# Kernel tuning notes

Hardware: AMD Instinct MI355X
Metric: run time of the kernel (lower is better)

The kernel has to match this reference:

```python
import jax, jax.numpy as jnp
import numpy as np
from jax import lax

# ---- static config (matches init_kwargs) ----
ORDER = 1
NPTS = ORDER + 1            # 2
JUNC_K = 300
LINE_K = 5000
NMS_SIZE = 3
JUNC_THRESH = 0.008
EPS = 1e-5
B, C, H, W = 4, 256, 160, 160
HID = C // 4                # 64
OUT_CH = [1, 1, 2, 1, 2, 4]  # lmap,jmap,joff,cmap,coff,lvec
NHEADS = len(OUT_CH)
MAXO = max(OUT_CH)          # pad conv2 out-channels to 4 per head
# channel-select indices from padded (NHEADS*MAXO) grouped-conv output
SEL = np.array([h * MAXO + c for h, k in enumerate(OUT_CH) for c in range(k)])
# lvec channel permutation from original forward (identity for order=1)
PERM = np.arange(OUT_CH[-1]).reshape(-1, 2, 2)
PERM[:, 1] = PERM[::-1, 1]
PERM = PERM.reshape(-1)


def setup_inputs() -> dict:
    key = jax.random.key(0)
    ks = jax.random.split(key, 9)
    features = jax.random.normal(ks[0], (B, C, H, W), jnp.float32)
    w1 = jax.random.normal(ks[1], (NHEADS * HID, C, 3, 3), jnp.float32) / np.sqrt(C * 9)
    b1 = 0.01 * jax.random.normal(ks[2], (NHEADS * HID,), jnp.float32)
    gamma = 1.0 + 0.1 * jax.random.normal(ks[3], (NHEADS * HID,), jnp.float32)
    beta = 0.01 * jax.random.normal(ks[4], (NHEADS * HID,), jnp.float32)
    mean = 0.1 * jax.random.normal(ks[5], (NHEADS * HID,), jnp.float32)
    var = jax.random.uniform(ks[6], (NHEADS * HID,), jnp.float32, 0.5, 1.5)
    w2 = jax.random.normal(ks[7], (NHEADS * MAXO, HID, 3, 3), jnp.float32) / np.sqrt(HID * 9)
    b2 = 0.01 * jax.random.normal(ks[8], (NHEADS * MAXO,), jnp.float32)
    return dict(features=features, w1=w1, b1=b1, gamma=gamma, beta=beta,
                mean=mean, var=var, w2=w2, b2=b2)


def _conv(x, w, b, groups=1):
    y = lax.conv_general_dilated(x, w, (1, 1), 'SAME',
                                 dimension_numbers=('NCHW', 'OIHW', 'NCHW'),
                                 feature_group_count=groups)
    return y + b[None, :, None, None]


def _nms(hm):  # hm: (1,H,W) -> suppress non-peaks
    mx = lax.reduce_window(hm, -jnp.inf, lax.max, (1, NMS_SIZE, NMS_SIZE),
                           (1, 1, 1), [(0, 0), (1, 1), (1, 1)])
    return jnp.where(hm == mx, hm, 0.0)


def _post(jm, joff, cm, coff, lv):
    """Per-sample postprocess. jm,cm:(1,H,W) joff,coff:(2,H,W) lv:(4,H,W).
    Returns (pts:(LINE_K,2,2) padded lines, mask:(LINE_K,) validity)."""
    # junctions: NMS + top-K + thresh mask + offset gather
    sj, ij = lax.top_k(_nms(jm).reshape(-1), JUNC_K)
    valid_j = sj >= JUNC_THRESH
    xy = jnp.stack([ij % W, ij // W], -1).astype(jm.dtype)
    junc = xy + joff.reshape(2, -1).T[ij] + 0.5
    junc = jnp.stack([jnp.clip(junc[:, 0], 0.0, W - 1e-4),
                      jnp.clip(junc[:, 1], 0.0, H - 1e-4)], -1)
    # lines: top-K centers + vector field gather (thresh=0 -> always full K)
    sc, ic = lax.top_k(cm.reshape(-1), LINE_K)
    cxy = jnp.stack([ic % W, ic // W], -1).astype(cm.dtype)
    center = cxy + coff.reshape(2, -1).T[ic] + 0.5
    lvr = lv.reshape(NPTS // 2 * 2, 2, -1).transpose(2, 0, 1)  # (HW,2,2)
    loi = center[:, None] + lvr[ic]                            # (L,2,2)
    loi = jnp.stack([jnp.clip(loi[..., 0], 0.0, W - 1e-4),
                     jnp.clip(loi[..., 1], 0.0, H - 1e-4)], -1)
    # pairwise squared-distance argmin of each endpoint to junctions
    d1 = ((loi[:, None, 0] - junc[None]) ** 2).sum(-1)
    d2 = ((loi[:, None, -1] - junc[None]) ** 2).sum(-1)
    big = jnp.asarray(1e18, d1.dtype)
    i1 = jnp.argmin(jnp.where(valid_j[None], d1, big), axis=-1)
    i2 = jnp.argmin(jnp.where(valid_j[None], d2, big), axis=-1)
    imin = jnp.minimum(i1, i2)
    imax = jnp.maximum(i1, i2)
    keep = imin != imax
    # unique (imin,imax) pairs via sorted-key dedup (matches torch.unique order)
    BIGK = JUNC_K * JUNC_K
    keyv = jnp.where(keep, imin * JUNC_K + imax, BIGK)
    sk = jnp.sort(keyv)
    first = jnp.concatenate([jnp.ones((1,), bool), sk[1:] != sk[:-1]]) & (sk < BIGK)
    a = jnp.where(first, sk // JUNC_K, 0)
    b = jnp.where(first, sk % JUNC_K, 0)
    pts = jnp.stack([junc[a], junc[b]], axis=1)  # (L,2,2)
    swap = pts[:, 0, 1] > pts[:, 1, 1]
    pts = jnp.where(swap[:, None, None], pts[:, ::-1], pts)
    return pts, first


def _maps(features, w1, b1, gamma, beta, mean, var, w2, b2):
    y = _conv(features, w1, b1)
    y = (y - mean[None, :, None, None]) * gamma[None, :, None, None] * \
        lax.rsqrt(var + EPS)[None, :, None, None] + beta[None, :, None, None]
    y = jax.nn.relu(y)
    y = _conv(y, w2, b2, groups=NHEADS)        # (B, NHEADS*MAXO, H, W)
    m = y[:, SEL]                              # (B, 11, H, W)
    lmap = jax.nn.sigmoid(m[:, 0:1])
    jmap = jax.nn.sigmoid(m[:, 1:2])
    joff = m[:, 2:4]
    cmap = jax.nn.sigmoid(m[:, 4:5])
    coff = m[:, 5:7]
    lvec = m[:, 7:][:, PERM]
    return lmap, jmap, joff, cmap, coff, lvec


def reference(features, w1, b1, gamma, beta, mean, var, w2, b2):
    lmap, jmap, joff, cmap, coff, lvec = _maps(features, w1, b1, gamma, beta,
                                               mean, var, w2, b2)
    loi, mask = jax.vmap(_post)(jmap, joff, cmap, coff, lvec)
    return lmap, jmap, joff, cmap, coff, lvec, loi, mask


if __name__ == '__main__':
    out = reference(**setup_inputs())
    for o in out:
        print(o.shape, o.dtype)
```

## Files before the change

kernel.cpp:

```cpp
#include <hip/hip_runtime.h>
#include <math.h>

#define IMG   160
#define HWSZ  25600
#define NB    4
#define CIN   256
#define COUT1 384
#define BIGK  90000

#define OFF_LMAP 0
#define OFF_JMAP 102400
#define OFF_JOFF 204800
#define OFF_CMAP 409600
#define OFF_COFF 512000
#define OFF_LVEC 716800
#define OFF_LOI  1126400
#define OFF_MASK 1206400

static const size_t WS_Y1    = 0;
static const size_t WS_JSORT = (size_t)NB * COUT1 * HWSZ * 4;
static const size_t WS_CSORT = WS_JSORT + (size_t)NB * 32768 * 8;
static const size_t WS_JUNC  = WS_CSORT + (size_t)NB * 32768 * 8;
static const size_t WS_JVAL  = WS_JUNC + (size_t)NB * 300 * 2 * 4;
static const size_t WS_LKEY  = WS_JVAL + (size_t)NB * 300 * 4;
static const size_t WS_WPK   = WS_LKEY + (size_t)NB * 8192 * 4;
static const size_t WS_FPK         = WS_WPK + (size_t)12 * 8 * 9 * 32 * 64 * 2;
static const size_t WS_NEED_LEGACY = WS_FPK;
static const size_t WS_NEED_PK     = WS_FPK + (size_t)NB * 8 * 162 * 162 * 128;

typedef unsigned long long u64;
typedef __attribute__((ext_vector_type(8))) short short8;
typedef __attribute__((ext_vector_type(4))) float f32x4;
typedef __attribute__((ext_vector_type(4))) int int4v;

union frag_u { short8 s8; u64 u[2]; int4v v; };

__device__ __forceinline__ float clip_coord(float v) {
    return fminf(fmaxf(v, 0.0f), 159.9999f);
}
__device__ __forceinline__ float sigmoidf(float v) {
    return 1.0f / (1.0f + expf(-v));
}
__device__ __forceinline__ unsigned short f2bf(float f) {
    unsigned u = __float_as_uint(f);
    return (unsigned short)((u + 0x7FFFu + ((u >> 16) & 1u)) >> 16);
}
__device__ __forceinline__ float bf2f(unsigned short h) {
    return __uint_as_float((unsigned)h << 16);
}

__device__ __forceinline__ void async_copy16(void* lds, const void* g) {
    __builtin_amdgcn_global_load_lds(
        (const __attribute__((address_space(1))) unsigned int*)g,
        (__attribute__((address_space(3))) unsigned int*)lds, 16, 0, 0);
}


__global__ void wpack_pk_kernel(const float* __restrict__ w1, short* __restrict__ wpk) {
    int e = blockIdx.x * 256 + threadIdx.x;
    int row = e >> 6, sp = e & 63;
    int ocl = row & 31;
    int tap = (row >> 5) % 9;
    int icc = (row / 288) & 7;
    int octile = row / 2304;
    int p16 = sp >> 3, j = sp & 7;
    int l16 = p16 ^ (ocl & 7);
    int ql = l16 * 8 + j;
    int term = ql >> 5, icl = ql & 31;
    int oc = octile * 32 + ocl, ic = icc * 32 + icl;
    float a = w1[((size_t)oc * CIN + ic) * 9 + tap];
    unsigned short hi = f2bf(a);
    wpk[e] = (term == 0) ? (short)hi : (short)f2bf(a - bf2f(hi));
}

__global__ __launch_bounds__(256) void pack_feat_kernel(
    const float* __restrict__ feat, short* __restrict__ fpk) {
    int e = blockIdx.x * 256 + threadIdx.x;
    int p = e & 7;
    int rest = e >> 3;
    int px = rest % 162;
    int t2 = rest / 162;
    int py = t2 % 162;
    int bi = t2 / 162;
    int s = (2 * py + px) & 7;
    int l = p ^ s;
    int term = l >> 2;
    int c0 = (l & 3) * 8;
    int gy = py - 1, gx = px - 1;
    bool valid = ((unsigned)gy < (unsigned)IMG) && ((unsigned)gx < (unsigned)IMG);
    const float* fs = feat + (size_t)(bi * 32 + c0) * HWSZ + (valid ? gy * IMG + gx : 0);
    unsigned d[4];
#pragma unroll
    for (int j2 = 0; j2 < 4; ++j2) {
        float va = valid ? fs[(size_t)(2 * j2) * HWSZ]     : 0.0f;
        float vb = valid ? fs[(size_t)(2 * j2 + 1) * HWSZ] : 0.0f;
        unsigned short ha = f2bf(va), hb = f2bf(vb);
        unsigned short oa = term ? f2bf(va - bf2f(ha)) : ha;
        unsigned short ob = term ? f2bf(vb - bf2f(hb)) : hb;
        d[j2] = (unsigned)oa | ((unsigned)ob << 16);
    }
    int4v o = { (int)d[0], (int)d[1], (int)d[2], (int)d[3] };
    *(int4v*)(fpk + (size_t)rest * 64 + p * 8) = o;
}

__global__ __launch_bounds__(256, 2) void conv1_mfma_pk(
    const short* __restrict__ fpk, const short* __restrict__ wpk,
    const float* __restrict__ b1, const float* __restrict__ gamma,
    const float* __restrict__ beta, const float* __restrict__ mean,
    const float* __restrict__ var, float* __restrict__ y1) {
    const int bid   = blockIdx.x;
    const int slot  = bid >> 3;
    const int tile  = (bid & 7) + ((slot / 12) << 3);
    const int octile = slot - (slot / 12) * 12;
    const int bb = tile / 100, tt = tile % 100;
    const int ty = (tt / 10) * 16, tx = (tt % 10) * 16;
    const int oc0 = octile * 32;
    const int tid  = threadIdx.x;
    const int w    = tid >> 6;
    const int lane = tid & 63;
    const int quad = lane >> 4;
    const int l15  = lane & 15;
    const int wbase = tid & 192;

    __shared__ __align__(16) short Alds[288 * 64];
    __shared__ __align__(16) short Blds[324 * 64];

    int aoff[2];
#pragma unroll
    for (int t = 0; t < 2; ++t)
        aoff[t] = l15 * 128 + ((((t << 2) | quad) ^ (l15 & 7)) << 4);

    f32x4 acc[2][4];
#pragma unroll
    for (int mi = 0; mi < 2; ++mi)
#pragma unroll
        for (int nj = 0; nj < 4; ++nj) acc[mi][nj] = (f32x4){0.f, 0.f, 0.f, 0.f};

    const char* asrc0 = (const char*)wpk + (size_t)(octile * 8) * 36864;

#pragma unroll 1
    for (int icc = 0; icc < 8; ++icc) {
        __syncthreads();
        {
            const char* asrc = asrc0 + (size_t)icc * 36864;
#pragma unroll
            for (int i = 0; i < 9; ++i) {
                int k = i * 256 + tid;
                async_copy16((char*)Alds + (size_t)(i * 256 + wbase) * 16,
                             asrc + (size_t)k * 16);
            }
        }
        {
            const char* bsrc = (const char*)fpk
                + (((size_t)(bb * 8 + icc) * 162 + ty) * 162 + tx) * 128;
#pragma unroll
            for (int it = 0; it < 10; ++it) {
                int k = it * 256 + tid;
                int hy = (int)((unsigned)k / 144u);
                int r  = k - hy * 144;
                async_copy16((char*)Blds + (size_t)(it * 256 + wbase) * 16,
                             bsrc + (size_t)hy * (162 * 128) + (size_t)r * 16);
            }
            if (tid < 32) {
                const int4v vv = *(const int4v*)(bsrc + (size_t)17 * (162 * 128)
                                                 + (size_t)(112 + tid) * 16);
                *(int4v*)((char*)Blds + (size_t)(2560 + tid) * 16) = vv;
            }
        }
        __syncthreads();

#pragma unroll
        for (int tap = 0; tap < 9; ++tap) {
            const int sy = tap / 3, sx = tap % 3;
            frag_u Af[2][2], Bf[2][4];
#pragma unroll
            for (int t = 0; t < 2; ++t) {
#pragma unroll
                for (int mi = 0; mi < 2; ++mi) {
                    const char* ap = (const char*)Alds
                        + (size_t)(tap * 32 + mi * 16) * 128 + aoff[t];
                    Af[t][mi].v = *(const int4v*)ap;
                }
#pragma unroll
                for (int nj = 0; nj < 4; ++nj) {
                    int pos = (w * 4 + nj + sy) * 18 + (l15 + sx);
                    const char* bp = (const char*)Blds + (size_t)pos * 128
                        + ((((t << 2) | quad) ^ (pos & 7)) << 4);
                    Bf[t][nj].v = *(const int4v*)bp;
                }
            }
#pragma unroll
            for (int mi = 0; mi < 2; ++mi)
#pragma unroll
                for (int nj = 0; nj < 4; ++nj) {
                    acc[mi][nj] = __builtin_amdgcn_mfma_f32_16x16x32_bf16(
                        Af[0][mi].s8, Bf[0][nj].s8, acc[mi][nj], 0, 0, 0);
                    acc[mi][nj] = __builtin_amdgcn_mfma_f32_16x16x32_bf16(
                        Af[0][mi].s8, Bf[1][nj].s8, acc[mi][nj], 0, 0, 0);
                    acc[mi][nj] = __builtin_amdgcn_mfma_f32_16x16x32_bf16(
                        Af[1][mi].s8, Bf[0][nj].s8, acc[mi][nj], 0, 0, 0);
                    acc[mi][nj] = __builtin_amdgcn_mfma_f32_16x16x32_bf16(
                        Af[1][mi].s8, Bf[1][nj].s8, acc[mi][nj], 0, 0, 0);
                }
        }
    }

#pragma unroll
    for (int nj = 0; nj < 4; ++nj) {
        const int gy = ty + w * 4 + nj, gx = tx + l15;
#pragma unroll
        for (int mi = 0; mi < 2; ++mi)
#pragma unroll
            for (int r = 0; r < 4; ++r) {
                const int oc = oc0 + mi * 16 + quad * 4 + r;
                float v = acc[mi][nj][r] + b1[oc];
                v = (v - mean[oc]) * (gamma[oc] / sqrtf(var[oc] + 1e-5f)) + beta[oc];
                y1[((size_t)(bb * COUT1 + oc)) * HWSZ + gy * IMG + gx] = fmaxf(v, 0.0f);
            }
    }
}


__global__ void wpack_kernel(const float* __restrict__ w1, short* __restrict__ wpk) {
    int e = blockIdx.x * 256 + threadIdx.x;
    int row = e >> 6, sp = e & 63;
    int ocl = row & 31;
    int tap = (row >> 5) % 9;
    int icc = (row / 288) & 7;
    int octile = row / 2304;
    int s = (sp >> 2) ^ (ocl & 15);
    int ql = s * 4 + (sp & 3);
    int term = ql >> 5, icl = ql & 31;
    int oc = octile * 32 + ocl, ic = icc * 32 + icl;
    float a = w1[((size_t)oc * CIN + ic) * 9 + tap];
    unsigned short hi = f2bf(a);
    wpk[e] = (term == 0) ? (short)hi : (short)f2bf(a - bf2f(hi));
}

__global__ __launch_bounds__(256, 2) void conv1_mfma(
    const float* __restrict__ feat, const short* __restrict__ wpk,
    const float* __restrict__ b1, const float* __restrict__ gamma,
    const float* __restrict__ beta, const float* __restrict__ mean,
    const float* __restrict__ var, float* __restrict__ y1) {
    const int bid   = blockIdx.x;
    const int slot  = bid >> 3;
    const int tile  = (bid & 7) + ((slot / 12) << 3);
    const int octile = slot - (slot / 12) * 12;
    const int bb = tile / 100, tt = tile % 100;
    const int ty = (tt / 10) * 16, tx = (tt % 10) * 16;
    const int oc0 = octile * 32;
    const int tid  = threadIdx.x;
    const int w    = tid >> 6;
    const int lane = tid & 63;
    const int quad = lane >> 4;
    const int l15  = lane & 15;

    __shared__ short Alds[288 * 64];
    __shared__ short Blds[324 * 68];

    int aoff[2][2];
#pragma unroll
    for (int t = 0; t < 2; ++t)
#pragma unroll
        for (int h = 0; h < 2; ++h)
            aoff[t][h] = l15 * 128 + (((t * 8 + quad * 2 + h) ^ l15) * 8);

    f32x4 acc[2][4];
#pragma unroll
    for (int mi = 0; mi < 2; ++mi)
#pragma unroll
        for (int nj = 0; nj < 4; ++nj) acc[mi][nj] = (f32x4){0.f, 0.f, 0.f, 0.f};

    const int4v* asrc_base = (const int4v*)wpk + (size_t)(octile * 8) * 2304;
    unsigned* Bd = (unsigned*)Blds;

    float pv0[21], pv1[21];

#pragma unroll
    for (int ii = 0; ii < 21; ++ii) {
        int i = tid + ii * 256;
        if (i < 5184) {
            int icp = i / 324, hp = i - icp * 324;
            int hy = hp / 18, hx = hp - hy * 18;
            int gy = ty + hy - 1, gx = tx + hx - 1;
            bool valid = ((unsigned)gy < IMG) && ((unsigned)gx < IMG);
            const float* fs = feat + ((size_t)(bb * CIN + icp * 2)) * HWSZ
                                   + (valid ? (gy * IMG + gx) : 0);
            pv0[ii] = valid ? fs[0]    : 0.0f;
            pv1[ii] = valid ? fs[HWSZ] : 0.0f;
        }
    }

#pragma unroll 1
    for (int icc = 0; icc < 8; ++icc) {
        __syncthreads();
        {
            const int4v* asrc = asrc_base + (size_t)icc * 2304;
            int4v* adst = (int4v*)Alds;
#pragma unroll
            for (int i = 0; i < 9; ++i)
                adst[tid + i * 256] = asrc[tid + i * 256];
        }
#pragma unroll
        for (int ii = 0; ii < 21; ++ii) {
            int i = tid + ii * 256;
            if (i < 5184) {
                int icp = i / 324, hp = i - icp * 324;
                float v0 = pv0[ii], v1 = pv1[ii];
                unsigned short h0 = f2bf(v0), h1 = f2bf(v1);
                unsigned short m0 = f2bf(v0 - bf2f(h0)), m1 = f2bf(v1 - bf2f(h1));
                Bd[hp * 34 + icp]      = (unsigned)h0 | ((unsigned)h1 << 16);
                Bd[hp * 34 + 16 + icp] = (unsigned)m0 | ((unsigned)m1 << 16);
            }
        }
        __syncthreads();

        if (icc < 7) {
#pragma unroll
            for (int ii = 0; ii < 21; ++ii) {
                int i = tid + ii * 256;
                if (i < 5184) {
                    int icp = i / 324, hp = i - icp * 324;
                    int hy = hp / 18, hx = hp - hy * 18;
                    int gy = ty + hy - 1, gx = tx + hx - 1;
                    bool valid = ((unsigned)gy < IMG) && ((unsigned)gx < IMG);
                    const float* fs = feat
                        + ((size_t)(bb * CIN + (icc + 1) * 32 + icp * 2)) * HWSZ
                        + (valid ? (gy * IMG + gx) : 0);
                    pv0[ii] = valid ? fs[0]    : 0.0f;
                    pv1[ii] = valid ? fs[HWSZ] : 0.0f;
                }
            }
        }

#pragma unroll
        for (int tap = 0; tap < 9; ++tap) {
            const int sy = tap / 3, sx = tap % 3;
            frag_u Af[2][2], Bf[2][4];
#pragma unroll
            for (int t = 0; t < 2; ++t) {
#pragma unroll
                for (int mi = 0; mi < 2; ++mi) {
                    const char* base = (const char*)Alds + (tap * 32 + mi * 16) * 128;
                    Af[t][mi].u[0] = *(const u64*)(base + aoff[t][0]);
                    Af[t][mi].u[1] = *(const u64*)(base + aoff[t][1]);
                }
#pragma unroll
                for (int nj = 0; nj < 4; ++nj) {
                    int pos = (w * 4 + nj + sy) * 18 + (l15 + sx);
                    const short* bp = &Blds[pos * 68 + t * 32 + quad * 8];
                    Bf[t][nj].u[0] = *(const u64*)bp;
                    Bf[t][nj].u[1] = *(const u64*)(bp + 4);
                }
            }
#pragma unroll
            for (int mi = 0; mi < 2; ++mi)
#pragma unroll
                for (int nj = 0; nj < 4; ++nj) {
                    acc[mi][nj] = __builtin_amdgcn_mfma_f32_16x16x32_bf16(
                        Af[0][mi].s8, Bf[0][nj].s8, acc[mi][nj], 0, 0, 0);
                    acc[mi][nj] = __builtin_amdgcn_mfma_f32_16x16x32_bf16(
                        Af[0][mi].s8, Bf[1][nj].s8, acc[mi][nj], 0, 0, 0);
                    acc[mi][nj] = __builtin_amdgcn_mfma_f32_16x16x32_bf16(
                        Af[1][mi].s8, Bf[0][nj].s8, acc[mi][nj], 0, 0, 0);
                    acc[mi][nj] = __builtin_amdgcn_mfma_f32_16x16x32_bf16(
                        Af[1][mi].s8, Bf[1][nj].s8, acc[mi][nj], 0, 0, 0);
                }
        }
    }

#pragma unroll
    for (int nj = 0; nj < 4; ++nj) {
        const int gy = ty + w * 4 + nj, gx = tx + l15;
#pragma unroll
        for (int mi = 0; mi < 2; ++mi)
#pragma unroll
            for (int r = 0; r < 4; ++r) {
                const int oc = oc0 + mi * 16 + quad * 4 + r;
                float v = acc[mi][nj][r] + b1[oc];
                v = (v - mean[oc]) * (gamma[oc] / sqrtf(var[oc] + 1e-5f)) + beta[oc];
                y1[((size_t)(bb * COUT1 + oc)) * HWSZ + gy * IMG + gx] = fmaxf(v, 0.0f);
            }
    }
}


__global__ __launch_bounds__(256, 2) void conv2_kernel(
    const float* __restrict__ y1, const float* __restrict__ w2,
    const float* __restrict__ b2, float* __restrict__ out) {
    const int KH[6]   = {1, 1, 2, 1, 2, 4};
    const int REG[6]  = {OFF_LMAP, OFF_JMAP, OFF_JOFF, OFF_CMAP, OFF_COFF, OFF_LVEC};
    const int SIGF[6] = {1, 1, 0, 1, 0, 0};

    const int bz = blockIdx.z;
    const int b  = bz / 6;
    const int h  = bz % 6;
    const int k  = KH[h];
    const int tx = blockIdx.x * 16, ty = blockIdx.y * 16;
    const int lx = threadIdx.x, ly = threadIdx.y;
    const int tid = ly * 16 + lx;

    __shared__ float tin[16][18][33];
    float acc[4] = {0.0f, 0.0f, 0.0f, 0.0f};

    const float* yb = y1 + ((size_t)(b * COUT1 + h * 64)) * HWSZ;

    for (int ic0 = 0; ic0 < 64; ic0 += 16) {
        __syncthreads();
        for (int i = tid; i < 5184; i += 256) {
            int c = i / 324, rem = i - c * 324;
            int r = rem / 18, col = rem - r * 18;
            int gy = ty - 1 + r, gx = tx - 1 + col;
            float v = 0.0f;
            if (gy >= 0 && gy < IMG && gx >= 0 && gx < IMG)
                v = yb[(size_t)(ic0 + c) * HWSZ + gy * IMG + gx];
            tin[c][r][col] = v;
        }
        __syncthreads();
#pragma unroll 4
        for (int c = 0; c < 16; ++c) {
            float n0 = tin[c][ly][lx],     n1 = tin[c][ly][lx + 1],     n2 = tin[c][ly][lx + 2];
            float n3 = tin[c][ly + 1][lx], n4 = tin[c][ly + 1][lx + 1], n5 = tin[c][ly + 1][lx + 2];
            float n6 = tin[c][ly + 2][lx], n7 = tin[c][ly + 2][lx + 1], n8 = tin[c][ly + 2][lx + 2];
#pragma unroll
            for (int o = 0; o < 4; ++o) {
                if (o < k) {
                    const float* wp = w2 + ((size_t)((h * 4 + o) * 64 + (ic0 + c))) * 9;
                    acc[o] = fmaf(n0, wp[0], fmaf(n1, wp[1], fmaf(n2, wp[2],
                             fmaf(n3, wp[3], fmaf(n4, wp[4], fmaf(n5, wp[5],
                             fmaf(n6, wp[6], fmaf(n7, wp[7], fmaf(n8, wp[8], acc[o])))))))));
                }
            }
        }
    }

    const int p = (ty + ly) * IMG + tx + lx;
    for (int o = 0; o < k; ++o) {
        float v = acc[o] + b2[h * 4 + o];
        if (SIGF[h]) v = sigmoidf(v);
        out[REG[h] + ((size_t)(b * k + o)) * HWSZ + p] = v;
    }
}

__global__ void nms_pack_kernel(const float* __restrict__ out,
                                u64* __restrict__ jsort,
                                u64* __restrict__ csort) {
    const int g = blockIdx.x;
    const int b = g / 100, q = g % 100;
    const int p = q * 256 + threadIdx.x;
    const float* jm = out + OFF_JMAP + (size_t)b * HWSZ;
    const float* cm = out + OFF_CMAP + (size_t)b * HWSZ;

    const int x = p % IMG, y = p / IMG;
    float v = jm[p];
    float mx = v;
#pragma unroll
    for (int dy = -1; dy <= 1; ++dy)
#pragma unroll
        for (int dx = -1; dx <= 1; ++dx) {
            int nx = x + dx, ny = y + dy;
            if (nx >= 0 && nx < IMG && ny >= 0 && ny < IMG)
                mx = fmaxf(mx, jm[ny * IMG + nx]);
        }
    float nmsv = (v == mx) ? v : 0.0f;

    u64 tagj = ((u64)__float_as_uint(nmsv) << 32)
             | (u64)(0xFFFFFFFFu - (unsigned)p);
    u64 tagc = ((u64)__float_as_uint(cm[p]) << 32)
             | (u64)(0xFFFFFFFFu - (unsigned)p);
    jsort[(size_t)b * 32768 + p] = tagj;
    csort[(size_t)b * 32768 + p] = tagc;
    if (q < 28) {
        int pp = 25600 + q * 256 + threadIdx.x;
        jsort[(size_t)b * 32768 + pp] = 0ull;
        csort[(size_t)b * 32768 + pp] = 0ull;
    }
}

__global__ __launch_bounds__(1024) void sort64_ldsA(u64* __restrict__ buf) {
    __shared__ u64 s[8192];
    const size_t base = (size_t)blockIdx.x * 8192;
    const int cbase = (blockIdx.x & 3) * 8192;
    for (int i = threadIdx.x; i < 8192; i += 1024) s[i] = buf[base + i];
    for (int k = 2; k <= 8192; k <<= 1)
        for (int j = k >> 1; j > 0; j >>= 1) {
            __syncthreads();
            for (int t = threadIdx.x; t < 4096; t += 1024) {
                int i = ((t & ~(j - 1)) << 1) | (t & (j - 1));
                int l = i | j;
                bool desc = (((i + cbase) & k) == 0);
                u64 x = s[i], y = s[l];
                if (desc ? (x < y) : (x > y)) { s[i] = y; s[l] = x; }
            }
        }
    __syncthreads();
    for (int i = threadIdx.x; i < 8192; i += 1024) buf[base + i] = s[i];
}

__global__ void sort64_gstep(u64* __restrict__ buf, int k, int j) {
    int t = blockIdx.x * 256 + threadIdx.x;
    int arr = t >> 14, p = t & 16383;
    int i = ((p & ~(j - 1)) << 1) | (p & (j - 1));
    int l = i | j;
    bool desc = ((i & k) == 0);
    u64* a = buf + (size_t)arr * 32768;
    u64 x = a[i], y = a[l];
    if (desc ? (x < y) : (x > y)) { a[i] = y; a[l] = x; }
}

__global__ __launch_bounds__(1024) void sort64_ldsB(u64* __restrict__ buf, int k) {
    __shared__ u64 s[8192];
    const size_t base = (size_t)blockIdx.x * 8192;
    const int cbase = (blockIdx.x & 3) * 8192;
    for (int i = threadIdx.x; i < 8192; i += 1024) s[i] = buf[base + i];
    for (int j = 4096; j > 0; j >>= 1) {
        __syncthreads();
        for (int t = threadIdx.x; t < 4096; t += 1024) {
            int i = ((t & ~(j - 1)) << 1) | (t & (j - 1));
            int l = i | j;
            bool desc = (((i + cbase) & k) == 0);
            u64 x = s[i], y = s[l];
            if (desc ? (x < y) : (x > y)) { s[i] = y; s[l] = x; }
        }
    }
    __syncthreads();
    for (int i = threadIdx.x; i < 8192; i += 1024) buf[base + i] = s[i];
}

__global__ __launch_bounds__(1024) void sort32_lds(int* __restrict__ buf) {
    __shared__ int s[8192];
    int* a = buf + (size_t)blockIdx.x * 8192;
    for (int i = threadIdx.x; i < 8192; i += 1024) s[i] = a[i];
    for (int k = 2; k <= 8192; k <<= 1)
        for (int j = k >> 1; j > 0; j >>= 1) {
            __syncthreads();
            for (int t = threadIdx.x; t < 4096; t += 1024) {
                int i = ((t & ~(j - 1)) << 1) | (t & (j - 1));
                int l = i | j;
                bool asc = ((i & k) == 0);
                int x = s[i], y = s[l];
                if (asc ? (x > y) : (x < y)) { s[i] = y; s[l] = x; }
            }
        }
    __syncthreads();
    for (int i = threadIdx.x; i < 8192; i += 1024) a[i] = s[i];
}

__global__ void junction_kernel(const u64* __restrict__ jsort,
                                const float* __restrict__ out,
                                float* __restrict__ junc, int* __restrict__ jvalid) {
    const int b = blockIdx.x;
    const int t = threadIdx.x;
    if (t >= 300) return;
    u64 key = jsort[(size_t)b * 32768 + t];
    float score  = __uint_as_float((unsigned)(key >> 32));
    unsigned idx = 0xFFFFFFFFu - (unsigned)(key & 0xFFFFFFFFull);
    const float* j0 = out + OFF_JOFF + (size_t)(b * 2) * HWSZ;
    const float* j1 = j0 + HWSZ;
    float jx = (float)(idx % IMG) + j0[idx] + 0.5f;
    float jy = (float)(idx / IMG) + j1[idx] + 0.5f;
    junc[(size_t)(b * 300 + t) * 2]     = clip_coord(jx);
    junc[(size_t)(b * 300 + t) * 2 + 1] = clip_coord(jy);
    jvalid[b * 300 + t] = (score >= 0.008f) ? 1 : 0;
}

__global__ void lines_kernel(const u64* __restrict__ csort,
                             const float* __restrict__ junc,
                             const int* __restrict__ jvalid,
                             const float* __restrict__ out,
                             int* __restrict__ lkeys) {
    const int b = blockIdx.y;
    const int t = blockIdx.x * 256 + threadIdx.x;

    __shared__ float jx[300], jy[300];
    __shared__ int jv[300];
    for (int i = threadIdx.x; i < 300; i += 256) {
        jx[i] = junc[(size_t)(b * 300 + i) * 2];
        jy[i] = junc[(size_t)(b * 300 + i) * 2 + 1];
        jv[i] = jvalid[b * 300 + i];
    }
    __syncthreads();

    if (t >= 8192) return;
    if (t >= 5000) { lkeys[b * 8192 + t] = 0x7FFFFFFF; return; }

    u64 key = csort[(size_t)b * 32768 + t];
    unsigned idx = 0xFFFFFFFFu - (unsigned)(key & 0xFFFFFFFFull);
    const float* c0 = out + OFF_COFF + (size_t)(b * 2) * HWSZ;
    const float* c1 = c0 + HWSZ;
    const float* lv = out + OFF_LVEC + (size_t)(b * 4) * HWSZ;

    float cx = (float)(idx % IMG) + c0[idx] + 0.5f;
    float cy = (float)(idx / IMG) + c1[idx] + 0.5f;
    float e0x = clip_coord(cx + lv[idx]);
    float e0y = clip_coord(cy + lv[HWSZ + idx]);
    float e1x = clip_coord(cx + lv[2 * HWSZ + idx]);
    float e1y = clip_coord(cy + lv[3 * HWSZ + idx]);

    float m1 = 1e18f, m2 = 1e18f;
    int i1 = 0, i2 = 0;
    for (int j = 0; j < 300; ++j) {
        if (jv[j]) {
            float dx = e0x - jx[j], dy = e0y - jy[j];
            float d = dx * dx + dy * dy;
            if (d < m1) { m1 = d; i1 = j; }
            dx = e1x - jx[j]; dy = e1y - jy[j];
            d = dx * dx + dy * dy;
            if (d < m2) { m2 = d; i2 = j; }
        }
    }
    int imin = min(i1, i2), imax = max(i1, i2);
    lkeys[b * 8192 + t] = (i1 != i2) ? (imin * 300 + imax) : BIGK;
}

__global__ void finalize_kernel(const int* __restrict__ lkeys,
                                const float* __restrict__ junc,
                                float* __restrict__ out) {
    const int b = blockIdx.y;
    const int t = blockIdx.x * 256 + threadIdx.x;
    if (t >= 5000) return;
    const int* lk = lkeys + b * 8192;
    int sk = lk[t];
    bool first = ((t == 0) || (sk != lk[t - 1])) && (sk < BIGK);
    int a  = first ? sk / 300 : 0;
    int bb = first ? sk % 300 : 0;
    float p0x = junc[(size_t)(b * 300 + a) * 2];
    float p0y = junc[(size_t)(b * 300 + a) * 2 + 1];
    float p1x = junc[(size_t)(b * 300 + bb) * 2];
    float p1y = junc[(size_t)(b * 300 + bb) * 2 + 1];
    if (p0y > p1y) {
        float tx = p0x; p0x = p1x; p1x = tx;
        float ty = p0y; p0y = p1y; p1y = ty;
    }
    size_t base = OFF_LOI + (size_t)(b * 5000 + t) * 4;
    out[base]     = p0x;
    out[base + 1] = p0y;
    out[base + 2] = p1x;
    out[base + 3] = p1y;
    out[OFF_MASK + b * 5000 + t] = first ? 1.0f : 0.0f;
}

extern "C" void kernel_launch(void* const* d_in, const int* in_sizes, int n_in,
                              void* d_out, int out_size, void* d_ws, size_t ws_size,
                              hipStream_t stream) {
    const float* feat  = (const float*)d_in[0];
    const float* w1    = (const float*)d_in[1];
    const float* b1    = (const float*)d_in[2];
    const float* gamma = (const float*)d_in[3];
    const float* beta  = (const float*)d_in[4];
    const float* mean  = (const float*)d_in[5];
    const float* var   = (const float*)d_in[6];
    const float* w2    = (const float*)d_in[7];
    const float* b2    = (const float*)d_in[8];
    float* out = (float*)d_out;
    char*  ws  = (char*)d_ws;

    if (ws_size < WS_NEED_LEGACY) return;

    float* y1 = (float*)(ws + WS_Y1);
    u64* jsort = (u64*)(ws + WS_JSORT);
    float* junc = (float*)(ws + WS_JUNC);
    int* jvalid = (int*)(ws + WS_JVAL);
    int* lkeys  = (int*)(ws + WS_LKEY);
    u64* csort = (u64*)(ws + WS_CSORT);
    short* wpk = (short*)(ws + WS_WPK);
    short* fpk = (short*)(ws + WS_FPK);

    if (ws_size >= WS_NEED_PK) {
        wpack_pk_kernel<<<dim3(6912), dim3(256), 0, stream>>>(w1, wpk);
        pack_feat_kernel<<<dim3(26244), dim3(256), 0, stream>>>(feat, fpk);
        conv1_mfma_pk<<<dim3(4800), dim3(256), 0, stream>>>(
            fpk, wpk, b1, gamma, beta, mean, var, y1);
    } else {
        wpack_kernel<<<dim3(6912), dim3(256), 0, stream>>>(w1, wpk);
        conv1_mfma<<<dim3(4800), dim3(256), 0, stream>>>(
            feat, wpk, b1, gamma, beta, mean, var, y1);
    }

    conv2_kernel<<<dim3(10, 10, NB * 6), dim3(16, 16), 0, stream>>>(y1, w2, b2, out);

    nms_pack_kernel<<<dim3(NB * 100), dim3(256), 0, stream>>>(out, jsort, csort);

    sort64_ldsA<<<dim3(32), dim3(1024), 0, stream>>>(jsort);
    sort64_gstep<<<dim3(512), dim3(256), 0, stream>>>(jsort, 16384, 8192);
    sort64_ldsB<<<dim3(32), dim3(1024), 0, stream>>>(jsort, 16384);
    sort64_gstep<<<dim3(512), dim3(256), 0, stream>>>(jsort, 32768, 16384);
    sort64_gstep<<<dim3(512), dim3(256), 0, stream>>>(jsort, 32768, 8192);
    sort64_ldsB<<<dim3(32), dim3(1024), 0, stream>>>(jsort, 32768);

    junction_kernel<<<dim3(NB), dim3(320), 0, stream>>>(jsort, out, junc, jvalid);

    lines_kernel<<<dim3(32, NB), dim3(256), 0, stream>>>(csort, junc, jvalid, out, lkeys);

    sort32_lds<<<dim3(NB), dim3(1024), 0, stream>>>(lkeys);

    finalize_kernel<<<dim3(20, NB), dim3(256), 0, stream>>>(lkeys, junc, out);
}
```

Measured before the change: 1.072 ms.

## Trim split-bf16 MFMA terms, reuse B fragments, and widen conv2 per-thread work

Conv1 drops the lo*lo cross term of the split-bf16 product, cutting MFMAs per tap from four to three. It also loads B fragments once per column shift and reuses them across the three row taps. The BN scale is precomputed by a tiny kernel instead of a divide and sqrt per output. Feature packing emits both hi and lo halves from one thread, halving global reads. Conv2 computes two horizontal pixels per thread with vector LDS reads and precomputed staging indices. Dropping the lo*lo term slightly reduces conv1 accuracy.

New measurement: 967.9 us. 1.11x faster.

```diff
diff --git a/kernel.cpp b/kernel.cpp
--- a/kernel.cpp
+++ b/kernel.cpp
@@ -24,9 +24,10 @@
 static const size_t WS_JVAL  = WS_JUNC + (size_t)NB * 300 * 2 * 4;
 static const size_t WS_LKEY  = WS_JVAL + (size_t)NB * 300 * 4;
 static const size_t WS_WPK   = WS_LKEY + (size_t)NB * 8192 * 4;
-static const size_t WS_FPK         = WS_WPK + (size_t)12 * 8 * 9 * 32 * 64 * 2;
-static const size_t WS_NEED_LEGACY = WS_FPK;
-static const size_t WS_NEED_PK     = WS_FPK + (size_t)NB * 8 * 162 * 162 * 128;
+static const size_t WS_NEED_LEGACY = WS_WPK + (size_t)12 * 8 * 9 * 32 * 64 * 2;
+static const size_t WS_BNS   = WS_NEED_LEGACY;
+static const size_t WS_FPK   = WS_BNS + 384 * 4;
+static const size_t WS_NEED_PK = WS_FPK + (size_t)NB * 8 * 162 * 162 * 128;
 
 typedef unsigned long long u64;
 typedef __attribute__((ext_vector_type(8))) short short8;
@@ -55,6 +56,13 @@
         (__attribute__((address_space(3))) unsigned int*)lds, 16, 0, 0);
 }
 
+
+__global__ void bnscale_kernel(const float* __restrict__ gamma,
+                               const float* __restrict__ var,
+                               float* __restrict__ bns) {
+    int i = blockIdx.x * 256 + threadIdx.x;
+    if (i < COUT1) bns[i] = gamma[i] / sqrtf(var[i] + 1e-5f);
+}
 
 __global__ void wpack_pk_kernel(const float* __restrict__ w1, short* __restrict__ wpk) {
     int e = blockIdx.x * 256 + threadIdx.x;
@@ -75,39 +83,41 @@
 
 __global__ __launch_bounds__(256) void pack_feat_kernel(
     const float* __restrict__ feat, short* __restrict__ fpk) {
-    int e = blockIdx.x * 256 + threadIdx.x;
-    int p = e & 7;
-    int rest = e >> 3;
-    int px = rest % 162;
-    int t2 = rest / 162;
-    int py = t2 % 162;
-    int bi = t2 / 162;
-    int s = (2 * py + px) & 7;
-    int l = p ^ s;
-    int term = l >> 2;
-    int c0 = (l & 3) * 8;
-    int gy = py - 1, gx = px - 1;
-    bool valid = ((unsigned)gy < (unsigned)IMG) && ((unsigned)gx < (unsigned)IMG);
-    const float* fs = feat + (size_t)(bi * 32 + c0) * HWSZ + (valid ? gy * IMG + gx : 0);
-    unsigned d[4];
+    const int tid = threadIdx.x;
+    const int c4  = (tid >> 4) & 3;
+    const int r0  = (tid & 15) | (((tid >> 6) & 3) << 4);
+    const int rest = blockIdx.x * 64 + r0;
+    const int px = rest % 162;
+    const int t2 = rest / 162;
+    const int py = t2 % 162;
+    const int bi = t2 / 162;
+    const int s  = (2 * py + px) & 7;
+    const int gy = py - 1, gx = px - 1;
+    const bool valid = ((unsigned)gy < (unsigned)IMG) && ((unsigned)gx < (unsigned)IMG);
+    const float* fs = feat + (size_t)(bi * 32 + c4 * 8) * HWSZ
+                           + (valid ? gy * IMG + gx : 0);
+    unsigned hi4[4], lo4[4];
 #pragma unroll
     for (int j2 = 0; j2 < 4; ++j2) {
         float va = valid ? fs[(size_t)(2 * j2) * HWSZ]     : 0.0f;
         float vb = valid ? fs[(size_t)(2 * j2 + 1) * HWSZ] : 0.0f;
         unsigned short ha = f2bf(va), hb = f2bf(vb);
-        unsigned short oa = term ? f2bf(va - bf2f(ha)) : ha;
-        unsigned short ob = term ? f2bf(vb - bf2f(hb)) : hb;
-        d[j2] = (unsigned)oa | ((unsigned)ob << 16);
-    }
-    int4v o = { (int)d[0], (int)d[1], (int)d[2], (int)d[3] };
-    *(int4v*)(fpk + (size_t)rest * 64 + p * 8) = o;
+        unsigned short la = f2bf(va - bf2f(ha)), lb = f2bf(vb - bf2f(hb));
+        hi4[j2] = (unsigned)ha | ((unsigned)hb << 16);
+        lo4[j2] = (unsigned)la | ((unsigned)lb << 16);
+    }
+    const int p0 = c4 ^ s;
+    const int p1 = (c4 | 4) ^ s;
+    int4v* base = (int4v*)(fpk + (size_t)rest * 64);
+    base[p0] = (int4v){ (int)hi4[0], (int)hi4[1], (int)hi4[2], (int)hi4[3] };
+    base[p1] = (int4v){ (int)lo4[0], (int)lo4[1], (int)lo4[2], (int)lo4[3] };
 }
 
 __global__ __launch_bounds__(256, 2) void conv1_mfma_pk(
     const short* __restrict__ fpk, const short* __restrict__ wpk,
-    const float* __restrict__ b1, const float* __restrict__ gamma,
+    const float* __restrict__ b1, const float* __restrict__ bns,
     const float* __restrict__ beta, const float* __restrict__ mean,
-    const float* __restrict__ var, float* __restrict__ y1) {
+    float* __restrict__ y1) {
     const int bid   = blockIdx.x;
     const int slot  = bid >> 3;
     const int tile  = (bid & 7) + ((slot / 12) << 3);
@@ -170,38 +180,41 @@
         __syncthreads();
 
 #pragma unroll
-        for (int tap = 0; tap < 9; ++tap) {
-            const int sy = tap / 3, sx = tap % 3;
-            frag_u Af[2][2], Bf[2][4];
-#pragma unroll
-            for (int t = 0; t < 2; ++t) {
-#pragma unroll
-                for (int mi = 0; mi < 2; ++mi) {
-                    const char* ap = (const char*)Alds
-                        + (size_t)(tap * 32 + mi * 16) * 128 + aoff[t];
-                    Af[t][mi].v = *(const int4v*)ap;
-                }
-#pragma unroll
-                for (int nj = 0; nj < 4; ++nj) {
-                    int pos = (w * 4 + nj + sy) * 18 + (l15 + sx);
+        for (int sx = 0; sx < 3; ++sx) {
+            frag_u Bf[2][6];
+#pragma unroll
+            for (int t = 0; t < 2; ++t)
+#pragma unroll
+                for (int rr = 0; rr < 6; ++rr) {
+                    int pos = (w * 4 + rr) * 18 + (l15 + sx);
                     const char* bp = (const char*)Blds + (size_t)pos * 128
                         + ((((t << 2) | quad) ^ (pos & 7)) << 4);
-                    Bf[t][nj].v = *(const int4v*)bp;
+                    Bf[t][rr].v = *(const int4v*)bp;
                 }
-            }
-#pragma unroll
-            for (int mi = 0; mi < 2; ++mi)
-#pragma unroll
-                for (int nj = 0; nj < 4; ++nj) {
-                    acc[mi][nj] = __builtin_amdgcn_mfma_f32_16x16x32_bf16(
-                        Af[0][mi].s8, Bf[0][nj].s8, acc[mi][nj], 0, 0, 0);
-                    acc[mi][nj] = __builtin_amdgcn_mfma_f32_16x16x32_bf16(
-                        Af[0][mi].s8, Bf[1][nj].s8, acc[mi][nj], 0, 0, 0);
-                    acc[mi][nj] = __builtin_amdgcn_mfma_f32_16x16x32_bf16(
-                        Af[1][mi].s8, Bf[0][nj].s8, acc[mi][nj], 0, 0, 0);
-                    acc[mi][nj] = __builtin_amdgcn_mfma_f32_16x16x32_bf16(
-                        Af[1][mi].s8, Bf[1][nj].s8, acc[mi][nj], 0, 0, 0);
-                }
+#pragma unroll
+            for (int sy = 0; sy < 3; ++sy) {
+                const int tap = sy * 3 + sx;
+                frag_u Af[2][2];
+#pragma unroll
+                for (int t = 0; t < 2; ++t)
+#pragma unroll
+                    for (int mi = 0; mi < 2; ++mi) {
+                        const char* ap = (const char*)Alds
+                            + (size_t)(tap * 32 + mi * 16) * 128 + aoff[t];
+                        Af[t][mi].v = *(const int4v*)ap;
+                    }
+#pragma unroll
+                for (int mi = 0; mi < 2; ++mi)
+#pragma unroll
+                    for (int nj = 0; nj < 4; ++nj) {
+                        acc[mi][nj] = __builtin_amdgcn_mfma_f32_16x16x32_bf16(
+                            Af[0][mi].s8, Bf[0][nj + sy].s8, acc[mi][nj], 0, 0, 0);
+                        acc[mi][nj] = __builtin_amdgcn_mfma_f32_16x16x32_bf16(
+                            Af[0][mi].s8, Bf[1][nj + sy].s8, acc[mi][nj], 0, 0, 0);
+                        acc[mi][nj] = __builtin_amdgcn_mfma_f32_16x16x32_bf16(
+                            Af[1][mi].s8, Bf[0][nj + sy].s8, acc[mi][nj], 0, 0, 0);
+                    }
+            }
         }
     }
 
@@ -214,7 +227,7 @@
             for (int r = 0; r < 4; ++r) {
                 const int oc = oc0 + mi * 16 + quad * 4 + r;
                 float v = acc[mi][nj][r] + b1[oc];
-                v = (v - mean[oc]) * (gamma[oc] / sqrtf(var[oc] + 1e-5f)) + beta[oc];
+                v = (v - mean[oc]) * bns[oc] + beta[oc];
                 y1[((size_t)(bb * COUT1 + oc)) * HWSZ + gy * IMG + gx] = fmaxf(v, 0.0f);
             }
     }
@@ -396,49 +409,86 @@
     const int b  = bz / 6;
     const int h  = bz % 6;
     const int k  = KH[h];
-    const int tx = blockIdx.x * 16, ty = blockIdx.y * 16;
+    const int tx = blockIdx.x * 32, ty = blockIdx.y * 16;
     const int lx = threadIdx.x, ly = threadIdx.y;
     const int tid = ly * 16 + lx;
 
-    __shared__ float tin[16][18][33];
-    float acc[4] = {0.0f, 0.0f, 0.0f, 0.0f};
+    __shared__ float tin[16][18][40];
+    float* const tinf = &tin[0][0][0];
+    float accv[4][2] = {{0.f,0.f},{0.f,0.f},{0.f,0.f},{0.f,0.f}};
 
     const float* yb = y1 + ((size_t)(b * COUT1 + h * 64)) * HWSZ;
+
+    bool sok[3], sval[3];
+    int  soff[3], sidx[3];
+#pragma unroll
+    for (int j = 0; j < 3; ++j) {
+        int idx = tid + j * 256;
+        sok[j] = (idx < 612);
+        int r = idx / 34, col = idx - r * 34;
+        int gy = ty - 1 + r, gx = tx - 1 + col;
+        sval[j] = sok[j] && ((unsigned)gy < (unsigned)IMG) && ((unsigned)gx < (unsigned)IMG);
+        soff[j] = sval[j] ? (gy * IMG + gx) : 0;
+        sidx[j] = r * 40 + col;
+    }
 
     for (int ic0 = 0; ic0 < 64; ic0 += 16) {
         __syncthreads();
-        for (int i = tid; i < 5184; i += 256) {
-            int c = i / 324, rem = i - c * 324;
-            int r = rem / 18, col = rem - r * 18;
-            int gy = ty - 1 + r, gx = tx - 1 + col;
-            float v = 0.0f;
-            if (gy >= 0 && gy < IMG && gx >= 0 && gx < IMG)
-                v = yb[(size_t)(ic0 + c) * HWSZ + gy * IMG + gx];
-            tin[c][r][col] = v;
+#pragma unroll
+        for (int j = 0; j < 3; ++j) {
+            if (sok[j]) {
+                const float* yp = yb + (size_t)ic0 * HWSZ + soff[j];
+                float* tp = tinf + sidx[j];
+#pragma unroll 4
+                for (int c = 0; c < 16; ++c)
+                    tp[c * 720] = sval[j] ? yp[(size_t)c * HWSZ] : 0.0f;
+            }
         }
         __syncthreads();
-#pragma unroll 4
+
+        const float* tb = tinf + ly * 40 + 2 * lx;
+#pragma unroll 2
         for (int c = 0; c < 16; ++c) {
-            float n0 = tin[c][ly][lx],     n1 = tin[c][ly][lx + 1],     n2 = tin[c][ly][lx + 2];
-            float n3 = tin[c][ly + 1][lx], n4 = tin[c][ly + 1][lx + 1], n5 = tin[c][ly + 1][lx + 2];
-            float n6 = tin[c][ly + 2][lx], n7 = tin[c][ly + 2][lx + 1], n8 = tin[c][ly + 2][lx + 2];
+            const float* tc = tb + c * 720;
+            float n[3][4];
+#pragma unroll
+            for (int r = 0; r < 3; ++r) {
+                float2 u = *(const float2*)(tc + r * 40);
+                float2 v = *(const float2*)(tc + r * 40 + 2);
+                n[r][0] = u.x; n[r][1] = u.y; n[r][2] = v.x; n[r][3] = v.y;
+            }
 #pragma unroll
             for (int o = 0; o < 4; ++o) {
                 if (o < k) {
                     const float* wp = w2 + ((size_t)((h * 4 + o) * 64 + (ic0 + c))) * 9;
-                    acc[o] = fmaf(n0, wp[0], fmaf(n1, wp[1], fmaf(n2, wp[2],
-                             fmaf(n3, wp[3], fmaf(n4, wp[4], fmaf(n5, wp[5],
-                             fmaf(n6, wp[6], fmaf(n7, wp[7], fmaf(n8, wp[8], acc[o])))))))));
+                    float a0 = accv[o][0], a1 = accv[o][1];
+#pragma unroll
+                    for (int r = 0; r < 3; ++r) {
+                        float w0 = wp[3*r], w1 = wp[3*r+1], w2v = wp[3*r+2];
+                        a0 = fmaf(n[r][0], w0, a0);
+                        a1 = fmaf(n[r][1], w0, a1);
+                        a0 = fmaf(n[r][1], w1, a0);
+                        a1 = fmaf(n[r][2], w1, a1);
+                        a0 = fmaf(n[r][2], w2v, a0);
+                        a1 = fmaf(n[r][3], w2v, a1);
+                    }
+                    accv[o][0] = a0; accv[o][1] = a1;
                 }
             }
         }
     }
 
-    const int p = (ty + ly) * IMG + tx + lx;
-    for (int o = 0; o < k; ++o) {
-        float v = acc[o] + b2[h * 4 + o];
-        if (SIGF[h]) v = sigmoidf(v);
-        out[REG[h] + ((size_t)(b * k + o)) * HWSZ + p] = v;
+    const int p = (ty + ly) * IMG + tx + 2 * lx;
+#pragma unroll
+    for (int o = 0; o < 4; ++o) {
+        if (o < k) {
+            float v0 = accv[o][0] + b2[h * 4 + o];
+            float v1 = accv[o][1] + b2[h * 4 + o];
+            if (SIGF[h]) { v0 = sigmoidf(v0); v1 = sigmoidf(v1); }
+            size_t base = (size_t)REG[h] + ((size_t)(b * k + o)) * HWSZ + p;
+            out[base]     = v0;
+            out[base + 1] = v1;
+        }
     }
 }
 
@@ -664,20 +714,22 @@
     int* lkeys  = (int*)(ws + WS_LKEY);
     u64* csort = (u64*)(ws + WS_CSORT);
     short* wpk = (short*)(ws + WS_WPK);
+    float* bns = (float*)(ws + WS_BNS);
     short* fpk = (short*)(ws + WS_FPK);
 
     if (ws_size >= WS_NEED_PK) {
         wpack_pk_kernel<<<dim3(6912), dim3(256), 0, stream>>>(w1, wpk);
-        pack_feat_kernel<<<dim3(26244), dim3(256), 0, stream>>>(feat, fpk);
+        bnscale_kernel<<<dim3(2), dim3(256), 0, stream>>>(gamma, var, bns);
+        pack_feat_kernel<<<dim3(13122), dim3(256), 0, stream>>>(feat, fpk);
         conv1_mfma_pk<<<dim3(4800), dim3(256), 0, stream>>>(
-            fpk, wpk, b1, gamma, beta, mean, var, y1);
+            fpk, wpk, b1, bns, beta, mean, y1);
     } else {
         wpack_kernel<<<dim3(6912), dim3(256), 0, stream>>>(w1, wpk);
         conv1_mfma<<<dim3(4800), dim3(256), 0, stream>>>(
             feat, wpk, b1, gamma, beta, mean, var, y1);
     }
 
-    conv2_kernel<<<dim3(10, 10, NB * 6), dim3(16, 16), 0, stream>>>(y1, w2, b2, out);
+    conv2_kernel<<<dim3(5, 10, NB * 6), dim3(16, 16), 0, stream>>>(y1, w2, b2, out);
 
     nms_pack_kernel<<<dim3(NB * 100), dim3(256), 0, stream>>>(out, jsort, csort);
 
```
